# Kernel tuning notes

Measured on AMD Instinct MI355X. Metric: run time of the kernel, lower is better.

Reference implementation:

```python
import jax, jax.numpy as jnp
import numpy as np

NUM_HEADS = 12
EPS = 1e-6


def softmax_with_policy(attn, policy, eps=EPS):
    # attn: [B, H, N, N]; policy: [B, N, 1]
    B, H, N, _ = attn.shape
    attn_policy = policy.reshape(B, 1, 1, N)
    eye = jnp.eye(N, dtype=attn_policy.dtype).reshape(1, 1, N, N)
    attn_policy = attn_policy + (1.0 - attn_policy) * eye
    max_att = jnp.max(attn, axis=-1, keepdims=True)
    a = jnp.exp((attn - max_att).astype(jnp.float32)) * attn_policy.astype(jnp.float32)
    a = (a + eps / N) / (jnp.sum(a, axis=-1, keepdims=True) + eps)
    return a.astype(attn.dtype)


def setup_inputs() -> dict:
    key = jax.random.key(0)
    k1, k2, k3 = jax.random.split(key, 3)
    B, N, C = 16, 1024, 768
    x = jax.random.normal(k1, (B, N, C), dtype=jnp.float32)
    policy = jax.random.uniform(k2, (B, N, 1), dtype=jnp.float32)
    w_qkv = jax.random.normal(k3, (3 * C, C), dtype=jnp.float32) * (C ** -0.5)
    w_proj = jax.random.normal(jax.random.fold_in(key, 7), (C, C), dtype=jnp.float32) * (C ** -0.5)
    b_proj = jnp.zeros((C,), dtype=jnp.float32)
    return {"x": x, "policy": policy, "w_qkv": w_qkv, "w_proj": w_proj, "b_proj": b_proj, "sampler": 0}


def reference(x, policy, w_qkv, w_proj, b_proj, sampler):
    B, N, C = x.shape
    H = NUM_HEADS
    hd = C // H
    scale = hd ** -0.5
    qkv = (x @ w_qkv.T).reshape(B, N, 3, H, hd)
    qkv = jnp.transpose(qkv, (2, 0, 3, 1, 4))  # [3, B, H, N, hd]
    q, k, v = qkv[0], qkv[1], qkv[2]
    attn = jnp.einsum('bhnd,bhmd->bhnm', q, k) * scale
    attn = softmax_with_policy(attn, policy)
    out = jnp.einsum('bhnm,bhmd->bhnd', attn, v)
    out = jnp.transpose(out, (0, 2, 1, 3)).reshape(B, N, C)
    return out @ w_proj.T + b_proj
```

## Files before the change

### kernel.cpp

```cpp
#include <hip/hip_runtime.h>


#define NB 16
#define NN 1024
#define NC 768
#define NH 12
#define HD 64
#define NM (NB*NN)
#define QKVC (3*NC)
#define QSCALE 0.18033688011112042f
#define PSTR 68

typedef _Float16 f16;
typedef _Float16 f16x8 __attribute__((ext_vector_type(8)));
typedef _Float16 f16x4 __attribute__((ext_vector_type(4)));
typedef __fp16 fp16x2 __attribute__((ext_vector_type(2)));
typedef float f32x4 __attribute__((ext_vector_type(4)));

#if __has_builtin(__builtin_amdgcn_exp2f)
#define EXP2(x) __builtin_amdgcn_exp2f(x)
#else
#define EXP2(x) exp2f(x)
#endif

#define MFMA16(a,b,c) __builtin_amdgcn_mfma_f32_16x16x32_f16((a),(b),(c),0,0,0)
#define SCHED_FENCE() __builtin_amdgcn_sched_barrier(0)

__device__ inline f16x8 as_f16x8(uint4 u){
  union { uint4 u; f16x8 h; } v; v.u = u; return v.h;
}

__device__ inline void gl_lds16(const f16* g, f16* l){
  __builtin_amdgcn_global_load_lds(
      (const __attribute__((address_space(1))) void*)g,
      (__attribute__((address_space(3))) void*)l, 16, 0, 0);
}

#define CVT_N1 (NM*NC/4)
#define CVT_N2 (QKVC*NC/4)
#define CVT_N3 (NC*NC/4)
__global__ void cvt_all(const float* __restrict__ x, const float* __restrict__ wq,
                        const float* __restrict__ wp, f16* __restrict__ xh,
                        f16* __restrict__ wqh, f16* __restrict__ wph){
  int i = blockIdx.x*blockDim.x + threadIdx.x;
  const float* in; f16* out; int j;
  if (i < CVT_N1){ in = x; out = xh; j = i; }
  else if (i < CVT_N1 + CVT_N2){ in = wq; out = wqh; j = i - CVT_N1; }
  else { in = wp; out = wph; j = i - CVT_N1 - CVT_N2; }
  float4 v = ((const float4*)in)[j];
  f16x4 h; h[0]=(f16)v.x; h[1]=(f16)v.y; h[2]=(f16)v.z; h[3]=(f16)v.w;
  ((f16x4*)out)[j] = h;
}

#define G_STAGE(SRC, DSTB, KT, RC0)                                           \
  _Pragma("unroll")                                                           \
  for (int j = 0; j < 4; j++){                                                \
    const int r_ = j*64 + (t >> 3);                                           \
    gl_lds16(SRC + (size_t)((RC0) + r_)*NC + (KT) + sslot*8,                  \
             (DSTB) + j*4096 + wv*512);                                       \
  }

#define GEMM256_PIPELINE(SRC_A, SRC_B)                                        \
  G_STAGE(SRC_A, sA, 0, R0);                                                  \
  G_STAGE(SRC_B, sB, 0, C0);                                                  \
  _Pragma("unroll 1")                                                         \
  for (int tt = 0; tt < 12; tt++){                                            \
    const int cur = tt & 1;                                                   \
    asm volatile("s_waitcnt vmcnt(0)" ::: "memory");      \
    SCHED_FENCE();                                                            \
    __builtin_amdgcn_s_barrier();                      \
    SCHED_FENCE();                                     \
    const f16* A_ = sA + (cur ? 16384 : 0);                                   \
    const f16* B_ = sB + (cur ? 16384 : 0);                                   \
    f16* An_ = sA + (cur ? 0 : 16384);                                        \
    f16* Bn_ = sB + (cur ? 0 : 16384);                                        \
    if (tt < 11){ G_STAGE(SRC_A, An_, (tt+1)*64, R0); }                       \
    {                                                                         \
      f16x8 bf[4];                                                            \
      _Pragma("unroll")                                                       \
      for (int nt = 0; nt < 4; nt++)                                          \
        bf[nt] = as_f16x8(*(const uint4*)(B_ + (wc*64 + nt*16 + lr)*64 + kxA0)); \
      __builtin_amdgcn_s_setprio(1);                                          \
      _Pragma("unroll")                                                       \
      for (int mt = 0; mt < 8; mt++){                                         \
        f16x8 af = as_f16x8(*(const uint4*)(A_ + (wr*128 + mt*16 + lr)*64 + kxA0)); \
        _Pragma("unroll")                                                     \
        for (int nt = 0; nt < 4; nt++)                                        \
          acc[mt][nt] = MFMA16(af, bf[nt], acc[mt][nt]);                      \
      }                                                                       \
      __builtin_amdgcn_s_setprio(0);                                          \
    }                                                                         \
    if (tt < 11){ G_STAGE(SRC_B, Bn_, (tt+1)*64, C0); }                       \
    {                                                                         \
      f16x8 bf[4];                                                            \
      _Pragma("unroll")                                                       \
      for (int nt = 0; nt < 4; nt++)                                          \
        bf[nt] = as_f16x8(*(const uint4*)(B_ + (wc*64 + nt*16 + lr)*64 + kxA1)); \
      __builtin_amdgcn_s_setprio(1);                                          \
      _Pragma("unroll")                                                       \
      for (int mt = 0; mt < 8; mt++){                                         \
        f16x8 af = as_f16x8(*(const uint4*)(A_ + (wr*128 + mt*16 + lr)*64 + kxA1)); \
        _Pragma("unroll")                                                     \
        for (int nt = 0; nt < 4; nt++)                                        \
          acc[mt][nt] = MFMA16(af, bf[nt], acc[mt][nt]);                      \
      }                                                                       \
      __builtin_amdgcn_s_setprio(0);                                          \
    }                                                                         \
  }

#define GEMM256_PREAMBLE                                                      \
  const int R0 = blockIdx.y*256, C0 = blockIdx.x*256;                         \
  const int t = threadIdx.x;                                                  \
  const int wv = t >> 6, l = t & 63, quad = l >> 4, lr = l & 15;              \
  const int wr = wv >> 2, wc = wv & 3;                                        \
  const int sslot = (t & 7) ^ ((t >> 3) & 7);                                 \
  const int xr = lr & 7;                                                      \
  const int kxA0 = (quad ^ xr)*8;                                             \
  const int kxA1 = ((4 + quad) ^ xr)*8;                                       \
  f32x4 acc[8][4] = {};

__launch_bounds__(512, 2)
__global__ void gemm_qkv(const f16* __restrict__ X, const f16* __restrict__ W,
                         f16* __restrict__ Q, f16* __restrict__ K, f16* __restrict__ VT){
  __shared__ f16 sA[2*16384];
  __shared__ f16 sB[2*16384];
  GEMM256_PREAMBLE;
  GEMM256_PIPELINE(X, W);
  const int type = C0 / NC;
#pragma unroll
  for (int nt = 0; nt < 4; nt++){
    int colg = C0 + wc*64 + nt*16 + lr;
    int rem  = colg - type*NC;
    int hh = rem >> 6, d = rem & 63;
#pragma unroll
    for (int mt = 0; mt < 8; mt++)
#pragma unroll
      for (int i = 0; i < 4; i++){
        int row = R0 + wr*128 + mt*16 + quad*4 + i;
        int bb = row >> 10, np = row & 1023;
        int bh = bb*NH + hh;
        float a = acc[mt][nt][i];
        if (type == 0)      Q[(bh << 16) + (np << 6) + d] = (f16)(a * QSCALE);
        else if (type == 1) K[(bh << 16) + (np << 6) + d] = (f16)a;
        else                VT[(bh << 16) + (d << 10) + np] = (f16)a;
      }
  }
}

__global__ void vsum_kernel(const f16* __restrict__ VT, float* __restrict__ vsum){
  int bh = blockIdx.x;
  int t = threadIdx.x;
  int row = t >> 2, part = t & 3;
  const uint4* p = (const uint4*)(VT + ((size_t)bh << 16) + row*NN + part*256);
  float s = 0.f;
#pragma unroll
  for (int i = 0; i < 32; i++){
    f16x8 v = as_f16x8(p[i]);
#pragma unroll
    for (int j = 0; j < 8; j++) s += (float)v[j];
  }
  __shared__ float sR[64][4];
  sR[row][part] = s;
  __syncthreads();
  if (t < 64) vsum[bh*64 + t] = sR[t][0] + sR[t][1] + sR[t][2] + sR[t][3];
}

#define STAGE(BUF, KEY0H)                                                     \
  _Pragma("unroll")                                                           \
  for (int j = 0; j < 2; j++){                                                \
    const int s_  = j*256 + t;                                                \
    const int r_  = s_ >> 3;                                                  \
    const int sl_ = (s_ & 7) ^ (r_ & 7);                                      \
    f16* du_ = (f16*)&sK[BUF][(j*256 + (t & 192))*8];                         \
    f16* dv_ = (f16*)&sVT[BUF][(j*256 + (t & 192))*8];                        \
    gl_lds16(Kg  + (size_t)((KEY0H) + r_)*HD + sl_*8, du_);                   \
    gl_lds16(VTg + (size_t)r_*NN + (KEY0H) + sl_*8,   dv_);                   \
  }

__launch_bounds__(256, 3)
__global__ void attn_kernel(const f16* __restrict__ Q, const f16* __restrict__ K,
                            const f16* __restrict__ VT, const float* __restrict__ policy,
                            const float* __restrict__ vsum, f16* __restrict__ O){
  __shared__ f16 sK[2][4096];
  __shared__ f16 sVT[2][4096];
  __shared__ f16 sP[4][2][16][PSTR];
  __shared__ float sPol[1024];

  const int blk = blockIdx.x;
  const int bh = blk % (NB*NH);
  const int qt = blk / (NB*NH);
  const int b = bh / NH;
  const size_t base = (size_t)bh << 16;

  const int t = threadIdx.x;
  const int w = t >> 6, l = t & 63, quad = l >> 4, lr = l & 15;
  const int q0 = qt*128 + w*32;
  const int qrow = q0 + lr;
  const int h = bh - b*NH;
  const int xr = lr & 7;
  const int kx0 = (quad ^ xr)*8;
  const int kx1 = ((4 + quad) ^ xr)*8;

  *(float4*)&sPol[t*4] = *(const float4*)(policy + b*NN + t*4);

  f16x8 qf[2][2];
#pragma unroll
  for (int tq = 0; tq < 2; tq++)
#pragma unroll
    for (int hf = 0; hf < 2; hf++)
      qf[tq][hf] = as_f16x8(*(const uint4*)(Q + base + (size_t)(q0 + tq*16 + lr)*HD + hf*32 + quad*8));

  float vs[4];
#pragma unroll
  for (int nt = 0; nt < 4; nt++) vs[nt] = vsum[bh*64 + nt*16 + lr];

  f16x8 ones;
#pragma unroll
  for (int j = 0; j < 8; j++) ones[j] = (f16)1.0f;

  float m_run[2] = {-INFINITY, -INFINITY};
  f32x4 acc_l[2] = {};
  f32x4 o[2][4] = {};

  const f16* Kg  = K + base;
  const f16* VTg = VT + base;

  STAGE(0, 0);
  asm volatile("s_waitcnt vmcnt(0) lgkmcnt(0)" ::: "memory");
  SCHED_FENCE();
  __builtin_amdgcn_s_barrier();
  SCHED_FENCE();

#pragma unroll 1
  for (int hs = 0; hs < 16; hs++){
    const int cur = hs & 1;
    const int key0h = hs*64;
    if (hs < 15){
      STAGE(cur^1, key0h + 64);
      asm volatile("s_waitcnt vmcnt(4)" ::: "memory");
    } else {
      asm volatile("s_waitcnt vmcnt(0)" ::: "memory");
    }
    SCHED_FENCE();
    __builtin_amdgcn_s_barrier();
    SCHED_FENCE();

    const f16* sKc = (const f16*)sK[cur];
    const f16* sVc = (const f16*)sVT[cur];

    f32x4 accA[4], accB[4];
#pragma unroll
    for (int ct = 0; ct < 4; ct++){ accA[ct] = (f32x4){0,0,0,0}; accB[ct] = (f32x4){0,0,0,0}; }
    __builtin_amdgcn_s_setprio(1);
#pragma unroll
    for (int ct = 0; ct < 4; ct++){
      const f16* kp = sKc + (ct*16 + lr)*64;
      f16x8 k0 = as_f16x8(*(const uint4*)(kp + kx0));
      f16x8 k1 = as_f16x8(*(const uint4*)(kp + kx1));
      accA[ct] = MFMA16(k0, qf[0][0], accA[ct]);
      accA[ct] = MFMA16(k1, qf[0][1], accA[ct]);
      accB[ct] = MFMA16(k0, qf[1][0], accB[ct]);
      accB[ct] = MFMA16(k1, qf[1][1], accB[ct]);
    }
    __builtin_amdgcn_s_setprio(0);

    {
      float mA = m_run[0], mB = m_run[1];
      const bool diag = (hs == 2*qt + (w >> 1));
      if (!diag){
#pragma unroll
        for (int ct = 0; ct < 4; ct++){
          const int kb = ct*16 + quad*4;
          float4 pol4 = *(const float4*)&sPol[key0h + kb];
          const float* p4 = (const float*)&pol4;
          mA = fmaxf(mA, fmaxf(fmaxf(accA[ct][0], accA[ct][1]), fmaxf(accA[ct][2], accA[ct][3])));
          mB = fmaxf(mB, fmaxf(fmaxf(accB[ct][0], accB[ct][1]), fmaxf(accB[ct][2], accB[ct][3])));
          union { f16x4 v; fp16x2 h[2]; } uA, uB;
          uA.h[0] = __builtin_amdgcn_cvt_pkrtz(EXP2(accA[ct][0])*p4[0], EXP2(accA[ct][1])*p4[1]);
          uA.h[1] = __builtin_amdgcn_cvt_pkrtz(EXP2(accA[ct][2])*p4[2], EXP2(accA[ct][3])*p4[3]);
          uB.h[0] = __builtin_amdgcn_cvt_pkrtz(EXP2(accB[ct][0])*p4[0], EXP2(accB[ct][1])*p4[1]);
          uB.h[1] = __builtin_amdgcn_cvt_pkrtz(EXP2(accB[ct][2])*p4[2], EXP2(accB[ct][3])*p4[3]);
          *(f16x4*)&sP[w][0][lr][kb] = uA.v;
          *(f16x4*)&sP[w][1][lr][kb] = uB.v;
        }
      } else {
#pragma unroll
        for (int ct = 0; ct < 4; ct++){
          const int kb = ct*16 + quad*4;
          float4 pol4 = *(const float4*)&sPol[key0h + kb];
          const float* p4 = (const float*)&pol4;
          float eA[4], eB[4];
#pragma unroll
          for (int i2 = 0; i2 < 4; i2++){
            int kg = key0h + kb + i2;
            float polA = (kg == qrow)      ? 1.0f : p4[i2];
            float polB = (kg == qrow + 16) ? 1.0f : p4[i2];
            mA = fmaxf(mA, accA[ct][i2]); mB = fmaxf(mB, accB[ct][i2]);
            eA[i2] = EXP2(accA[ct][i2]) * polA;
            eB[i2] = EXP2(accB[ct][i2]) * polB;
          }
          union { f16x4 v; fp16x2 h[2]; } uA, uB;
          uA.h[0] = __builtin_amdgcn_cvt_pkrtz(eA[0], eA[1]);
          uA.h[1] = __builtin_amdgcn_cvt_pkrtz(eA[2], eA[3]);
          uB.h[0] = __builtin_amdgcn_cvt_pkrtz(eB[0], eB[1]);
          uB.h[1] = __builtin_amdgcn_cvt_pkrtz(eB[2], eB[3]);
          *(f16x4*)&sP[w][0][lr][kb] = uA.v;
          *(f16x4*)&sP[w][1][lr][kb] = uB.v;
        }
      }
      m_run[0] = mA; m_run[1] = mB;
    }

    __builtin_amdgcn_s_setprio(1);
#pragma unroll
    for (int s8g = 0; s8g < 2; s8g++){
      f16x8 pfA = as_f16x8(*(const uint4*)&sP[w][0][lr][s8g*32 + quad*8]);
      f16x8 pfB = as_f16x8(*(const uint4*)&sP[w][1][lr][s8g*32 + quad*8]);
      acc_l[0] = MFMA16(pfA, ones, acc_l[0]);
      acc_l[1] = MFMA16(pfB, ones, acc_l[1]);
      const int sx = ((s8g*4 + quad) ^ xr)*8;
#pragma unroll
      for (int nt = 0; nt < 4; nt++){
        f16x8 vf = as_f16x8(*(const uint4*)(sVc + (nt*16 + lr)*64 + sx));
        o[0][nt] = MFMA16(pfA, vf, o[0][nt]);
        o[1][nt] = MFMA16(pfB, vf, o[1][nt]);
      }
    }
    __builtin_amdgcn_s_setprio(0);
    SCHED_FENCE();
    __builtin_amdgcn_s_barrier();
    SCHED_FENCE();
  }

#pragma unroll
  for (int tq = 0; tq < 2; tq++){
    float mq = m_run[tq];
    mq = fmaxf(mq, __shfl_xor(mq, 16));
    mq = fmaxf(mq, __shfl_xor(mq, 32));
#pragma unroll
    for (int i = 0; i < 4; i++){
      float mi = __shfl(mq, quad*4 + i);
      float E  = EXP2(mi);
      float li = acc_l[tq][i];
      float inv = 1.0f / (li + 1e-6f*E);
      float ec  = (1e-6f/1024.0f)*E;
      int row = q0 + tq*16 + quad*4 + i;
      f16* op = O + (size_t)(b*NN + row)*NC + h*HD;
#pragma unroll
      for (int nt = 0; nt < 4; nt++)
        op[nt*16 + lr] = (f16)((o[tq][nt][i] + ec*vs[nt]) * inv);
    }
  }
}

__launch_bounds__(512, 2)
__global__ void gemm_proj(const f16* __restrict__ A, const f16* __restrict__ W,
                          const float* __restrict__ bias, float* __restrict__ out){
  __shared__ f16 sA[2*16384];
  __shared__ f16 sB[2*16384];
  GEMM256_PREAMBLE;
  GEMM256_PIPELINE(A, W);
#pragma unroll
  for (int nt = 0; nt < 4; nt++){
    int colg = C0 + wc*64 + nt*16 + lr;
    float bv = bias[colg];
#pragma unroll
    for (int mt = 0; mt < 8; mt++)
#pragma unroll
      for (int i = 0; i < 4; i++){
        int row = R0 + wr*128 + mt*16 + quad*4 + i;
        out[(size_t)row*NC + colg] = acc[mt][nt][i] + bv;
      }
  }
}

extern "C" void kernel_launch(void* const* d_in, const int* in_sizes, int n_in,
                              void* d_out, int out_size, void* d_ws, size_t ws_size,
                              hipStream_t stream) {
  const float* x      = (const float*)d_in[0];
  const float* policy = (const float*)d_in[1];
  const float* w_qkv  = (const float*)d_in[2];
  const float* w_proj = (const float*)d_in[3];
  const float* b_proj = (const float*)d_in[4];
  float* out = (float*)d_out;

  f16* x_h     = (f16*)d_ws;
  f16* wqkv_h  = x_h + (size_t)NM*NC;
  f16* wproj_h = wqkv_h + (size_t)QKVC*NC;
  f16* q_h     = wproj_h + (size_t)NC*NC;
  f16* k_h     = q_h + (size_t)NM*NC;
  f16* vt_h    = k_h + (size_t)NM*NC;
  float* vsum_f = (float*)(vt_h + (size_t)NM*NC);
  f16* attn_h  = x_h;

  cvt_all<<<(CVT_N1+CVT_N2+CVT_N3)/256, 256, 0, stream>>>(x, w_qkv, w_proj, x_h, wqkv_h, wproj_h);

  gemm_qkv<<<dim3(QKVC/256, NM/256), 512, 0, stream>>>(x_h, wqkv_h, q_h, k_h, vt_h);

  vsum_kernel<<<dim3(NB*NH), 256, 0, stream>>>(vt_h, vsum_f);

  attn_kernel<<<dim3(NB*NH*(NN/128)), 256, 0, stream>>>(q_h, k_h, vt_h, policy, vsum_f, attn_h);

  gemm_proj<<<dim3(NC/256, NM/256), 512, 0, stream>>>(attn_h, wproj_h, b_proj, out);
}
```

Before: 348.1 us.

## Split GEMM main loop into four barrier-synchronized phases and remap workgroups across XCDs

Restructures the shared 256x256 GEMM main loop into four phases. Each phase loads a subset of A/B fragments from LDS, issues part of the next tile's global-to-LDS staging, then runs 16 MFMAs between workgroup barriers, in a ping-pong style meant to interleave memory and matrix work across waves. It also remaps the flat block index so consecutive blocks land on the same XCD, to improve L2 locality for the QKV and projection GEMMs. This adds barriers and explicit lgkmcnt waits that could add sync stalls, and the remap assumes the block count is divisible by 8.

```diff
diff --git a/kernel.cpp b/kernel.cpp
--- a/kernel.cpp
+++ b/kernel.cpp
@@ -52,64 +52,95 @@
   ((f16x4*)out)[j] = h;
 }
 
-#define G_STAGE(SRC, DSTB, KT, RC0)                                           \
+#define G_STAGE1(SRC, DSTB, KT, RC0, J)                                       \
+  gl_lds16(SRC + (size_t)((RC0) + (J)*64 + (t >> 3))*NC + (KT) + sslot*8,     \
+           (DSTB) + (J)*4096 + wv*512);
+
+#define G_STAGE4(SRC, DSTB, KT, RC0)                                          \
+  { G_STAGE1(SRC, DSTB, KT, RC0, 0) G_STAGE1(SRC, DSTB, KT, RC0, 1)           \
+    G_STAGE1(SRC, DSTB, KT, RC0, 2) G_STAGE1(SRC, DSTB, KT, RC0, 3) }
+
+#define PH_READ_BF(KX)                                                        \
   _Pragma("unroll")                                                           \
-  for (int j = 0; j < 4; j++){                                                \
-    const int r_ = j*64 + (t >> 3);                                           \
-    gl_lds16(SRC + (size_t)((RC0) + r_)*NC + (KT) + sslot*8,                  \
-             (DSTB) + j*4096 + wv*512);                                       \
-  }
+  for (int nt = 0; nt < 4; nt++)                                              \
+    bf[nt] = as_f16x8(*(const uint4*)(B_ + (wc*64 + nt*16 + lr)*64 + (KX)));
+
+#define PH_READ_AF(M0, KX)                                                    \
+  _Pragma("unroll")                                                           \
+  for (int mt = 0; mt < 4; mt++)                                              \
+    af[mt] = as_f16x8(*(const uint4*)(A_ + (wr*128 + ((M0)+mt)*16 + lr)*64 + (KX)));
+
+#define PH_MFMA(M0)                                                           \
+  asm volatile("s_waitcnt lgkmcnt(0)" ::: "memory");                          \
+  SCHED_FENCE();                                                              \
+  __builtin_amdgcn_s_setprio(1);                                              \
+  _Pragma("unroll")                                                           \
+  for (int mt = 0; mt < 4; mt++)                                              \
+    _Pragma("unroll")                                                         \
+    for (int nt = 0; nt < 4; nt++)                                            \
+      acc[(M0)+mt][nt] = MFMA16(af[mt], bf[nt], acc[(M0)+mt][nt]);            \
+  __builtin_amdgcn_s_setprio(0);                                              \
+  SCHED_FENCE();
 
 #define GEMM256_PIPELINE(SRC_A, SRC_B)                                        \
-  G_STAGE(SRC_A, sA, 0, R0);                                                  \
-  G_STAGE(SRC_B, sB, 0, C0);                                                  \
+  G_STAGE4(SRC_A, sA, 0, R0);                                                 \
+  G_STAGE4(SRC_B, sB, 0, C0);                                                 \
   _Pragma("unroll 1")                                                         \
   for (int tt = 0; tt < 12; tt++){                                            \
     const int cur = tt & 1;                                                   \
-    asm volatile("s_waitcnt vmcnt(0)" ::: "memory");      \
-    SCHED_FENCE();                                                            \
-    __builtin_amdgcn_s_barrier();                      \
-    SCHED_FENCE();                                     \
+    const int kn = (tt + 1)*64;                                               \
+    const bool st = (tt < 11);                                                \
+    asm volatile("s_waitcnt vmcnt(0)" ::: "memory");    \
+    SCHED_FENCE();                                                            \
+    __builtin_amdgcn_s_barrier();                       \
+    SCHED_FENCE();                                                            \
     const f16* A_ = sA + (cur ? 16384 : 0);                                   \
     const f16* B_ = sB + (cur ? 16384 : 0);                                   \
     f16* An_ = sA + (cur ? 0 : 16384);                                        \
     f16* Bn_ = sB + (cur ? 0 : 16384);                                        \
-    if (tt < 11){ G_STAGE(SRC_A, An_, (tt+1)*64, R0); }                       \
-    {                                                                         \
-      f16x8 bf[4];                                                            \
-      _Pragma("unroll")                                                       \
-      for (int nt = 0; nt < 4; nt++)                                          \
-        bf[nt] = as_f16x8(*(const uint4*)(B_ + (wc*64 + nt*16 + lr)*64 + kxA0)); \
-      __builtin_amdgcn_s_setprio(1);                                          \
-      _Pragma("unroll")                                                       \
-      for (int mt = 0; mt < 8; mt++){                                         \
-        f16x8 af = as_f16x8(*(const uint4*)(A_ + (wr*128 + mt*16 + lr)*64 + kxA0)); \
-        _Pragma("unroll")                                                     \
-        for (int nt = 0; nt < 4; nt++)                                        \
-          acc[mt][nt] = MFMA16(af, bf[nt], acc[mt][nt]);                      \
-      }                                                                       \
-      __builtin_amdgcn_s_setprio(0);                                          \
-    }                                                                         \
-    if (tt < 11){ G_STAGE(SRC_B, Bn_, (tt+1)*64, C0); }                       \
-    {                                                                         \
-      f16x8 bf[4];                                                            \
-      _Pragma("unroll")                                                       \
-      for (int nt = 0; nt < 4; nt++)                                          \
-        bf[nt] = as_f16x8(*(const uint4*)(B_ + (wc*64 + nt*16 + lr)*64 + kxA1)); \
-      __builtin_amdgcn_s_setprio(1);                                          \
-      _Pragma("unroll")                                                       \
-      for (int mt = 0; mt < 8; mt++){                                         \
-        f16x8 af = as_f16x8(*(const uint4*)(A_ + (wr*128 + mt*16 + lr)*64 + kxA1)); \
-        _Pragma("unroll")                                                     \
-        for (int nt = 0; nt < 4; nt++)                                        \
-          acc[mt][nt] = MFMA16(af, bf[nt], acc[mt][nt]);                      \
-      }                                                                       \
-      __builtin_amdgcn_s_setprio(0);                                          \
-    }                                                                         \
-  }
-
-#define GEMM256_PREAMBLE                                                      \
-  const int R0 = blockIdx.y*256, C0 = blockIdx.x*256;                         \
+    f16x8 af[4], bf[4];                                                       \
+                                              \
+    PH_READ_BF(kxA0); PH_READ_AF(0, kxA0);                                    \
+    SCHED_FENCE();                                                            \
+    if (st){ G_STAGE1(SRC_A, An_, kn, R0, 0) G_STAGE1(SRC_A, An_, kn, R0, 1) }\
+    SCHED_FENCE();                                                            \
+    __builtin_amdgcn_s_barrier();                                             \
+    PH_MFMA(0);                                                               \
+    __builtin_amdgcn_s_barrier();                                             \
+    SCHED_FENCE();                                                            \
+                                              \
+    PH_READ_AF(4, kxA0);                                                      \
+    SCHED_FENCE();                                                            \
+    if (st){ G_STAGE1(SRC_A, An_, kn, R0, 2) G_STAGE1(SRC_A, An_, kn, R0, 3) }\
+    SCHED_FENCE();                                                            \
+    __builtin_amdgcn_s_barrier();                                             \
+    PH_MFMA(4);                                                               \
+    __builtin_amdgcn_s_barrier();                                             \
+    SCHED_FENCE();                                                            \
+                                              \
+    PH_READ_BF(kxA1); PH_READ_AF(0, kxA1);                                    \
+    SCHED_FENCE();                                                            \
+    if (st){ G_STAGE1(SRC_B, Bn_, kn, C0, 0) G_STAGE1(SRC_B, Bn_, kn, C0, 1) }\
+    SCHED_FENCE();                                                            \
+    __builtin_amdgcn_s_barrier();                                             \
+    PH_MFMA(0);                                                               \
+    __builtin_amdgcn_s_barrier();                                             \
+    SCHED_FENCE();                                                            \
+                                              \
+    PH_READ_AF(4, kxA1);                                                      \
+    SCHED_FENCE();                                                            \
+    if (st){ G_STAGE1(SRC_B, Bn_, kn, C0, 2) G_STAGE1(SRC_B, Bn_, kn, C0, 3) }\
+    SCHED_FENCE();                                                            \
+    __builtin_amdgcn_s_barrier();                                             \
+    PH_MFMA(4);                                                               \
+    __builtin_amdgcn_s_barrier();                                             \
+    SCHED_FENCE();                                                            \
+  }
+
+#define GEMM256_PREAMBLE(NBX, NWG)                                            \
+  const int flat_ = blockIdx.y*(NBX) + blockIdx.x;                            \
+  const int wg_ = (flat_ % 8)*((NWG)/8) + flat_/8;                            \
+  const int R0 = (wg_/(NBX))*256, C0 = (wg_%(NBX))*256;                       \
   const int t = threadIdx.x;                                                  \
   const int wv = t >> 6, l = t & 63, quad = l >> 4, lr = l & 15;              \
   const int wr = wv >> 2, wc = wv & 3;                                        \
@@ -124,7 +155,7 @@
                          f16* __restrict__ Q, f16* __restrict__ K, f16* __restrict__ VT){
   __shared__ f16 sA[2*16384];
   __shared__ f16 sB[2*16384];
-  GEMM256_PREAMBLE;
+  GEMM256_PREAMBLE(9, 576);
   GEMM256_PIPELINE(X, W);
   const int type = C0 / NC;
 #pragma unroll
@@ -358,7 +389,7 @@
                           const float* __restrict__ bias, float* __restrict__ out){
   __shared__ f16 sA[2*16384];
   __shared__ f16 sB[2*16384];
-  GEMM256_PREAMBLE;
+  GEMM256_PREAMBLE(3, 192);
   GEMM256_PIPELINE(A, W);
 #pragma unroll
   for (int nt = 0; nt < 4; nt++){
```

Result: no change. 343.2 us (-1.4%).
